# Optimization experiments

Hardware: AMD Instinct MI355X
Metric: run time of the kernel (lower is better)

## Reference

```python
import jax, jax.numpy as jnp
import numpy as np

B, S, D = 4, 2048, 1024
E, K, H = 8, 2, 2048  # experts, top_k, swiglu hidden (ff_multiplier=2.0)
EPS = 1e-8
RMS_EPS = 1e-6
ROPE_BASE = 10000.0


def setup_inputs() -> dict:
    key = jax.random.key(0)
    ks = jax.random.split(key, 6)
    scale_in = 1.0 / np.sqrt(D)
    scale_h = 1.0 / np.sqrt(H)
    return {
        "x": jax.random.normal(ks[0], (B, S, D), jnp.float32),
        "norm_w": jnp.ones((D,), jnp.float32),
        "router_W": jax.random.normal(ks[1], (E, D), jnp.float32) * scale_in,  # nn.Linear weight [E,D]
        "w1": jax.random.normal(ks[2], (E, H, D), jnp.float32) * scale_in,  # gate proj per expert
        "w3": jax.random.normal(ks[3], (E, H, D), jnp.float32) * scale_in,  # up proj per expert
        "w2": jax.random.normal(ks[4], (E, D, H), jnp.float32) * scale_h,   # down proj per expert
    }


def _rmsnorm(x, w):
    var = jnp.mean(jnp.square(x), axis=-1, keepdims=True)
    return x * jax.lax.rsqrt(var + RMS_EPS) * w


def _rope(x):
    # half-split rotary embedding over full embed dim; x: [B,S,D]
    d2 = D // 2
    inv_freq = 1.0 / (ROPE_BASE ** (jnp.arange(0, d2, dtype=jnp.float32) / d2))
    ang = jnp.arange(S, dtype=jnp.float32)[:, None] * inv_freq[None, :]  # [S,D/2]
    cos, sin = jnp.cos(ang), jnp.sin(ang)
    x1, x2 = x[..., :d2], x[..., d2:]
    return jnp.concatenate([x1 * cos - x2 * sin, x1 * sin + x2 * cos], axis=-1)


def reference(x, norm_w, router_W, w1, w3, w2):
    hidden = _rope(_rmsnorm(x, norm_w))  # [B,S,D]
    logits = jnp.einsum("bsd,ed->bse", hidden, router_W)
    probs = jax.nn.softmax(logits, axis=-1)
    # sparse top-k renormalized gates
    top_v, top_i = jax.lax.top_k(probs, K)  # [B,S,K]
    sparse = jnp.sum(jax.nn.one_hot(top_i, E, dtype=probs.dtype) * top_v[..., None], axis=-2)  # [B,S,E]
    gates = sparse / jnp.clip(jnp.sum(sparse, axis=-1, keepdims=True), EPS)
    # dense all-expert SwiGLU
    g = jnp.einsum("bsd,ehd->bseh", hidden, w1)
    u = jnp.einsum("bsd,ehd->bseh", hidden, w3)
    act = jax.nn.silu(g) * u
    expert_out = jnp.einsum("bseh,edh->bsed", act, w2)  # [B,S,E,D]
    mixed = jnp.sum(gates[..., None] * expert_out, axis=-2)
    return mixed + x
```

## Files before the change

kernel.cpp:

```cpp
#include <hip/hip_runtime.h>

#define TOKENS 8192
#define Dm 1024
#define Hm 2048
#define Sm 2048
#define D2 512
#define SLOTS 16384
#define PADU 256
#define SLOTPAD (SLOTS + 8*PADU)
#define NWE 16777216

#define OF_TAB 0ull
#define OF_HID (OF_TAB + (size_t)Sm*D2*8)
#define OF_ACT (OF_HID + (size_t)TOKENS*Dm*2)
#define OF_W1B (OF_ACT + (size_t)SLOTPAD*Hm*2)
#define OF_W3B (OF_W1B + (size_t)NWE*2)
#define OF_W2B (OF_W3B + (size_t)NWE*2)
#define OF_T2I (OF_W2B + (size_t)NWE*2)
#define OF_T2G (OF_T2I + (size_t)TOKENS*2*4)
#define OF_T2S (OF_T2G + (size_t)TOKENS*2*4)
#define OF_ST  (OF_T2S + (size_t)TOKENS*2*4)
#define OF_SG  (OF_ST + (size_t)SLOTPAD*4)
#define OF_MT  (OF_SG + (size_t)SLOTPAD*4)
#define OF_SO  (OF_MT + 1024)

#define PREP_TOKEN 8192
#define PREP_CONV  (PREP_TOKEN + 3 * (NWE / (256 * 8)))
#define PREP_INIT  (PREP_CONV + (SLOTPAD + 255) / 256)

typedef __bf16 bf16x8 __attribute__((ext_vector_type(8)));
typedef short  s16x8  __attribute__((ext_vector_type(8)));
typedef float  f32x4  __attribute__((ext_vector_type(4)));

__device__ __forceinline__ unsigned short f2bf(float f) {
    union { float f; unsigned u; } v; v.f = f;
    unsigned r = v.u + 0x7fffu + ((v.u >> 16) & 1u);
    return (unsigned short)(r >> 16);
}

__device__ __forceinline__ float bf2f(unsigned short u) {
    union { unsigned u; float f; } v; v.u = ((unsigned)u) << 16;
    return v.f;
}

__device__ __forceinline__ f32x4 mfma16(s16x8 a, s16x8 b, f32x4 c) {
    return __builtin_amdgcn_mfma_f32_16x16x32_bf16(
        __builtin_bit_cast(bf16x8, a), __builtin_bit_cast(bf16x8, b), c, 0, 0, 0);
}

__device__ __forceinline__ void gld16(const void* g, void* l) {
    __builtin_amdgcn_global_load_lds(
        (const __attribute__((address_space(1))) void*)g,
        (__attribute__((address_space(3))) void*)l, 16, 0, 0);
}

__device__ __forceinline__ int xcd_swz(int bid, int nwg) {
    int cpx = nwg >> 3;
    return (bid & 7) * cpx + (bid >> 3);
}

__global__ __launch_bounds__(256) void k_prep(
    const float* __restrict__ x, const float* __restrict__ nw,
    const float* __restrict__ rW,
    const float* __restrict__ w1, const float* __restrict__ w3,
    const float* __restrict__ w2,
    unsigned short* __restrict__ hid, int* __restrict__ t2i,
    float* __restrict__ t2g,
    unsigned short* __restrict__ d1, unsigned short* __restrict__ d3,
    unsigned short* __restrict__ d2,
    int* __restrict__ slot_token, int* __restrict__ meta)
{
    __shared__ float red[4];
    __shared__ float rl[4][8];
    int bid = blockIdx.x;
    int tid = threadIdx.x;

    if (bid >= PREP_CONV) {
        int i = (bid - PREP_CONV) * 256 + tid;
        if (i < SLOTPAD) slot_token[i] = -1;
        if (i < 8) meta[i] = 0;
        return;
    }
    if (bid >= PREP_TOKEN) {
        size_t i = ((size_t)(bid - PREP_TOKEN) * 256 + tid) * 8;
        const float* s; unsigned short* d;
        if (i < (size_t)NWE)            { s = w1; d = d1; }
        else if (i < 2ull * NWE)        { s = w3; d = d3; i -= (size_t)NWE; }
        else                            { s = w2; d = d2; i -= 2ull * NWE; }
        float4 a = *(const float4*)(s + i);
        float4 b = *(const float4*)(s + i + 4);
        s16x8 v;
        v[0]=(short)f2bf(a.x); v[1]=(short)f2bf(a.y); v[2]=(short)f2bf(a.z); v[3]=(short)f2bf(a.w);
        v[4]=(short)f2bf(b.x); v[5]=(short)f2bf(b.y); v[6]=(short)f2bf(b.z); v[7]=(short)f2bf(b.w);
        *(s16x8*)(d + i) = v;
        return;
    }

    int t = bid;
    int lane = tid & 63, wid = tid >> 6;
    int s = t & (Sm - 1);
    const float* xr = x + (size_t)t * Dm;

    float v0 = xr[tid], v1 = xr[tid + 256], v2 = xr[tid + 512], v3 = xr[tid + 768];
    float ss = v0*v0 + v1*v1 + v2*v2 + v3*v3;
    #pragma unroll
    for (int o = 32; o; o >>= 1) ss += __shfl_down(ss, o);
    if (lane == 0) red[wid] = ss;
    __syncthreads();
    float tot = red[0] + red[1] + red[2] + red[3];
    float rms = rsqrtf(tot * (1.0f / Dm) + 1e-6f);

    float n0 = v0 * rms * nw[tid];
    float n1 = v1 * rms * nw[tid + 256];
    float n2 = v2 * rms * nw[tid + 512];
    float n3 = v3 * rms * nw[tid + 768];

    const float kk = -0.017988946039016842f;
    float a0 = (float)s * expf((float)tid * kk);
    float a1 = (float)s * expf((float)(tid + 256) * kk);
    float c0x = cosf(a0), c0y = sinf(a0);
    float c1x = cosf(a1), c1y = sinf(a1);
    float h0 = n0 * c0x - n2 * c0y;
    float h2 = n0 * c0y + n2 * c0x;
    float h1 = n1 * c1x - n3 * c1y;
    float h3 = n1 * c1y + n3 * c1x;

    size_t base = (size_t)t * Dm;
    hid[base + tid]       = f2bf(h0);
    hid[base + tid + 256] = f2bf(h1);
    hid[base + tid + 512] = f2bf(h2);
    hid[base + tid + 768] = f2bf(h3);

    float p[8];
    #pragma unroll
    for (int e = 0; e < 8; e++) {
        const float* r = rW + (size_t)e * Dm;
        p[e] = h0 * r[tid] + h1 * r[tid + 256] + h2 * r[tid + 512] + h3 * r[tid + 768];
    }
    #pragma unroll
    for (int e = 0; e < 8; e++)
        #pragma unroll
        for (int o = 32; o; o >>= 1) p[e] += __shfl_down(p[e], o);
    if (lane == 0) {
        #pragma unroll
        for (int e = 0; e < 8; e++) rl[wid][e] = p[e];
    }
    __syncthreads();
    if (tid == 0) {
        float lg[8];
        #pragma unroll
        for (int e = 0; e < 8; e++) lg[e] = rl[0][e] + rl[1][e] + rl[2][e] + rl[3][e];
        float m = lg[0];
        #pragma unroll
        for (int e = 1; e < 8; e++) m = fmaxf(m, lg[e]);
        int i0 = 0; float b0 = lg[0];
        #pragma unroll
        for (int e = 1; e < 8; e++) if (lg[e] > b0) { b0 = lg[e]; i0 = e; }
        int i1 = -1; float b1 = -3.0e38f;
        #pragma unroll
        for (int e = 0; e < 8; e++) if (e != i0 && lg[e] > b1) { b1 = lg[e]; i1 = e; }
        float p0 = expf(b0 - m), p1 = expf(b1 - m);
        float inv = 1.0f / (p0 + p1);
        t2i[2 * t] = i0; t2i[2 * t + 1] = i1;
        t2g[2 * t] = p0 * inv; t2g[2 * t + 1] = p1 * inv;
    }
}

__global__ __launch_bounds__(256) void k_hist(const int* __restrict__ t2i,
                                              int* __restrict__ meta) {
    __shared__ int h[8];
    int tid = threadIdx.x;
    if (tid < 8) h[tid] = 0;
    __syncthreads();
    int base = blockIdx.x * 512 + tid * 2;
    atomicAdd(&h[t2i[base]], 1);
    atomicAdd(&h[t2i[base + 1]], 1);
    __syncthreads();
    if (tid < 8) atomicAdd(&meta[tid], h[tid]);
}

__global__ void k_offsets(int* meta) {
    if (threadIdx.x == 0 && blockIdx.x == 0) {
        int acc = 0;
        for (int e = 0; e < 8; e++) {
            meta[8 + e] = acc;
            acc += ((meta[e] + PADU - 1) / PADU) * PADU;
        }
        meta[16] = acc;
        for (int e = 0; e < 8; e++) meta[17 + e] = meta[8 + e];
    }
}

__global__ __launch_bounds__(256) void k_place(
    const int* __restrict__ t2i, const float* __restrict__ t2g,
    int* __restrict__ slot_token, float* __restrict__ slot_gate,
    int* __restrict__ t2s, int* __restrict__ meta)
{
    __shared__ int lcnt[8];
    __shared__ int lbase[8];
    int tid = threadIdx.x;
    if (tid < 8) lcnt[tid] = 0;
    __syncthreads();
    int t = blockIdx.x * 256 + tid;
    int e0 = t2i[2 * t], e1 = t2i[2 * t + 1];
    int r0 = atomicAdd(&lcnt[e0], 1);
    int r1 = atomicAdd(&lcnt[e1], 1);
    __syncthreads();
    if (tid < 8) lbase[tid] = atomicAdd(&meta[17 + tid], lcnt[tid]);
    __syncthreads();
    int p0 = lbase[e0] + r0, p1 = lbase[e1] + r1;
    slot_token[p0] = t; slot_gate[p0] = t2g[2 * t];     t2s[2 * t]     = p0;
    slot_token[p1] = t; slot_gate[p1] = t2g[2 * t + 1]; t2s[2 * t + 1] = p1;
}

__global__ __launch_bounds__(512) void k_gemm1(
    const unsigned short* __restrict__ hid,
    const unsigned short* __restrict__ w1b, const unsigned short* __restrict__ w3b,
    const int* __restrict__ slot_token, unsigned short* __restrict__ act,
    const int* __restrict__ meta)
{
    int nwg = gridDim.x * gridDim.y;
    int bid = blockIdx.y * gridDim.x + blockIdx.x;
    int wg  = xcd_swz(bid, nwg);
    int bx  = wg % gridDim.x, by = wg / gridDim.x;

    int row0 = by * 256;
    if (row0 >= meta[16]) return;
    int e = 0;
    #pragma unroll
    for (int q = 1; q < 8; q++) if (row0 >= meta[8 + q]) e = q;
    int h0 = bx * 128;

    __shared__ unsigned short As[2][256 * 64];
    __shared__ unsigned short Bs[2][256 * 64];

    int tid = threadIdx.x, lane = tid & 63, w = tid >> 6;
    int wm = w >> 2, wn = w & 3;
    int wrow = wm * 128, wcol = wn * 32;
    int frow = lane & 15, q4 = lane >> 4;
    int rx = frow & 7;

    int grow = tid >> 3;
    int sslot = (tid & 7) ^ (grow & 7);

    const unsigned short* srcA[4];
    const unsigned short* srcB[4];
    #pragma unroll
    for (int g = 0; g < 4; g++) {
        int ra = g * 64 + grow;
        int tok = slot_token[row0 + ra];  if (tok < 0) tok = 0;
        srcA[g] = hid + (size_t)tok * Dm + sslot * 8;
        int rb = g * 64 + grow;
        srcB[g] = (rb < 128 ? w1b + ((size_t)e * Hm + h0 + rb) * Dm
                            : w3b + ((size_t)e * Hm + h0 + rb - 128) * Dm) + sslot * 8;
    }

    s16x8 a8[4][2], bG[2][2], bU[2][2];
    f32x4 accG[8][2] = {};
    f32x4 accU[8][2] = {};

#define SA(nb, g) gld16(srcA[g] + koff, (unsigned short*)&As[(nb)][(g) * 4096 + tid * 8])
#define SB(nb, g) gld16(srcB[g] + koff, (unsigned short*)&Bs[(nb)][(g) * 4096 + tid * 8])

#define RD_A(buf, half) do {                                                  \
    _Pragma("unroll") for (int i_ = 0; i_ < 4; i_++)                          \
    _Pragma("unroll") for (int kh_ = 0; kh_ < 2; kh_++) {                     \
        int sp_ = ((kh_ << 2) | q4) ^ rx;                                     \
        a8[i_][kh_] = *(const s16x8*)&As[(buf)][(wrow + (half) * 64 + i_ * 16 + frow) * 64 + sp_ * 8]; \
    } } while (0)

#define RD_B(buf, arr, base) do {                                             \
    _Pragma("unroll") for (int j_ = 0; j_ < 2; j_++)                          \
    _Pragma("unroll") for (int kh_ = 0; kh_ < 2; kh_++) {                     \
        int sp_ = ((kh_ << 2) | q4) ^ rx;                                     \
        arr[j_][kh_] = *(const s16x8*)&Bs[(buf)][((base) + wcol + j_ * 16 + frow) * 64 + sp_ * 8]; \
    } } while (0)

#define MFMA_Q(accX, bX, half) do {                                           \
    _Pragma("unroll") for (int i_ = 0; i_ < 4; i_++)                          \
    _Pragma("unroll") for (int j_ = 0; j_ < 2; j_++)                          \
    _Pragma("unroll") for (int kh_ = 0; kh_ < 2; kh_++)                       \
        accX[(half) * 4 + i_][j_] = mfma16(a8[i_][kh_], bX[j_][kh_], accX[(half) * 4 + i_][j_]); \
    } while (0)

#define PH_PRE  do { __builtin_amdgcn_s_barrier();                            \
    asm volatile("s_waitcnt lgkmcnt(0)" ::: "memory");                        \
    __builtin_amdgcn_sched_barrier(0);                                        \
    __builtin_amdgcn_s_setprio(1); } while (0)
#define PH_POST do { __builtin_amdgcn_s_setprio(0);                           \
    __builtin_amdgcn_s_barrier(); } while (0)

    {
        int koff = 0;
        #pragma unroll
        for (int g = 0; g < 4; g++) SA(0, g);
        #pragma unroll
        for (int g = 0; g < 4; g++) SB(0, g);
        asm volatile("s_waitcnt vmcnt(0)" ::: "memory");
        __builtin_amdgcn_s_barrier();
    }

    for (int kt = 0; kt < 16; ++kt) {
        int buf = kt & 1, nbuf = buf ^ 1;
        int koff = (kt + 1) * 64;
        bool st = kt < 15;
        RD_A(buf, 0); RD_B(buf, bG, 0);
        if (st) { SA(nbuf, 0); SA(nbuf, 1); SA(nbuf, 2); }
        PH_PRE; MFMA_Q(accG, bG, 0); PH_POST;
        RD_B(buf, bU, 128);
        if (st) { SA(nbuf, 3); SB(nbuf, 0); SB(nbuf, 1); }
        PH_PRE; MFMA_Q(accU, bU, 0); PH_POST;
        RD_A(buf, 1);
        if (st) { SB(nbuf, 2); SB(nbuf, 3); }
        PH_PRE; MFMA_Q(accG, bG, 1); PH_POST;
        __builtin_amdgcn_s_setprio(1);
        MFMA_Q(accU, bU, 1);
        __builtin_amdgcn_s_setprio(0);
        asm volatile("s_waitcnt vmcnt(0)" ::: "memory");
        __builtin_amdgcn_s_barrier();
        __builtin_amdgcn_sched_barrier(0);
    }

#undef SA
#undef SB
#undef RD_A
#undef RD_B
#undef MFMA_Q
#undef PH_PRE
#undef PH_POST

    #pragma unroll
    for (int m = 0; m < 8; m++)
        #pragma unroll
        for (int j = 0; j < 2; j++)
            #pragma unroll
            for (int r = 0; r < 4; r++) {
                int sr = row0 + wrow + m * 16 + q4 * 4 + r;
                int hc = h0 + wcol + j * 16 + frow;
                float g = accG[m][j][r], u = accU[m][j][r];
                float a = g / (1.0f + expf(-g)) * u;
                act[(size_t)sr * Hm + hc] = f2bf(a);
            }
}

__global__ __launch_bounds__(256) void k_gemm2(
    const unsigned short* __restrict__ act, const unsigned short* __restrict__ w2b,
    const float* __restrict__ slot_gate,
    unsigned short* __restrict__ sout, const int* __restrict__ meta)
{
    int nwg = gridDim.x * gridDim.y;
    int bid = blockIdx.y * gridDim.x + blockIdx.x;
    int wg  = xcd_swz(bid, nwg);
    int bx  = wg % gridDim.x, by = wg / gridDim.x;

    int row0 = by * 128;
    if (row0 >= meta[16]) return;
    int e = 0;
    #pragma unroll
    for (int q = 1; q < 8; q++) if (row0 >= meta[8 + q]) e = q;
    int d0 = bx * 128;

    __shared__ unsigned short As[2][128 * 64];
    __shared__ unsigned short Bs[2][128 * 64];
    __shared__ float sgat[128];

    int tid = threadIdx.x, lane = tid & 63, w = tid >> 6;
    int wm = w >> 1, wn = w & 1;
    int frow = lane & 15, q4 = lane >> 4;
    int rx = frow & 7;

    if (tid < 128) sgat[tid] = slot_gate[row0 + tid];

    int r7 = (tid >> 3) & 7;
    int sslot = (tid & 7) ^ r7;

    const unsigned short* srcA[4];
    const unsigned short* srcB[4];
    #pragma unroll
    for (int i = 0; i < 4; i++) {
        int rr = i * 32 + (tid >> 3);
        srcA[i] = act + (size_t)(row0 + rr) * Hm + sslot * 8;
        srcB[i] = w2b + ((size_t)e * Dm + d0 + rr) * Hm + sslot * 8;
    }

    f32x4 acc[4][4] = {};

#define STAGE2(buf, k0) do {                                                  \
    unsigned short* la_ = &As[(buf)][tid * 8];                                \
    unsigned short* lb_ = &Bs[(buf)][tid * 8];                                \
    _Pragma("unroll")                                                         \
    for (int i_ = 0; i_ < 4; i_++) {                                          \
        gld16(srcA[i_] + (k0), la_ + i_ * 2048);                              \
        gld16(srcB[i_] + (k0), lb_ + i_ * 2048);                              \
    } } while (0)

#define COMP2(buf) do {                                                       \
    _Pragma("unroll")                                                         \
    for (int h_ = 0; h_ < 2; h_++) {                                          \
        int sp_ = ((h_ << 2) | q4) ^ rx;                                      \
        s16x8 am_[4], bn_[4];                                                 \
        _Pragma("unroll")                                                     \
        for (int i_ = 0; i_ < 4; i_++)                                        \
            am_[i_] = *(const s16x8*)&As[(buf)][(wm * 64 + i_ * 16 + frow) * 64 + sp_ * 8]; \
        _Pragma("unroll")                                                     \
        for (int j_ = 0; j_ < 4; j_++)                                        \
            bn_[j_] = *(const s16x8*)&Bs[(buf)][(wn * 64 + j_ * 16 + frow) * 64 + sp_ * 8]; \
        _Pragma("unroll")                                                     \
        for (int i_ = 0; i_ < 4; i_++)                                        \
            _Pragma("unroll")                                                 \
            for (int j_ = 0; j_ < 4; j_++)                                    \
                acc[i_][j_] = mfma16(am_[i_], bn_[j_], acc[i_][j_]);          \
    } } while (0)

    STAGE2(0, 0);
    #pragma unroll 2
    for (int kt = 0; kt < 31; ++kt) {
        STAGE2((kt + 1) & 1, (kt + 1) * 64);
        asm volatile("s_waitcnt vmcnt(8)" ::: "memory");
        __builtin_amdgcn_s_barrier();
        __builtin_amdgcn_sched_barrier(0);
        COMP2(kt & 1);
        __builtin_amdgcn_sched_barrier(0);
        __builtin_amdgcn_s_barrier();
    }
    asm volatile("s_waitcnt vmcnt(0)" ::: "memory");
    __builtin_amdgcn_s_barrier();
    __builtin_amdgcn_sched_barrier(0);
    COMP2(1);

#undef STAGE2
#undef COMP2

    #pragma unroll
    for (int i = 0; i < 4; i++) {
        #pragma unroll
        for (int r = 0; r < 4; r++) {
            int srl = wm * 64 + i * 16 + q4 * 4 + r;
            float gate = sgat[srl];
            size_t rb = (size_t)(row0 + srl) * Dm;
            #pragma unroll
            for (int j = 0; j < 4; j++) {
                int dc = d0 + wn * 64 + j * 16 + frow;
                sout[rb + dc] = f2bf(gate * acc[i][j][r]);
            }
        }
    }
}

__global__ __launch_bounds__(256) void k_final(
    const float* __restrict__ x, const unsigned short* __restrict__ sout,
    const int* __restrict__ t2s, float* __restrict__ out)
{
    int t = blockIdx.x;
    int tid = threadIdx.x;
    int s0 = t2s[2 * t], s1 = t2s[2 * t + 1];
    const float4*  xr = (const float4*)(x + (size_t)t * Dm);
    const ushort4* a  = (const ushort4*)(sout + (size_t)s0 * Dm);
    const ushort4* b  = (const ushort4*)(sout + (size_t)s1 * Dm);
    float4* o = (float4*)(out + (size_t)t * Dm);
    float4 xv = xr[tid];
    ushort4 av = a[tid], bv = b[tid];
    float4 r;
    r.x = xv.x + bf2f(av.x) + bf2f(bv.x);
    r.y = xv.y + bf2f(av.y) + bf2f(bv.y);
    r.z = xv.z + bf2f(av.z) + bf2f(bv.z);
    r.w = xv.w + bf2f(av.w) + bf2f(bv.w);
    o[tid] = r;
}

extern "C" void kernel_launch(void* const* d_in, const int* in_sizes, int n_in,
                              void* d_out, int out_size, void* d_ws, size_t ws_size,
                              hipStream_t stream) {
    const float* x  = (const float*)d_in[0];
    const float* nw = (const float*)d_in[1];
    const float* rW = (const float*)d_in[2];
    const float* w1 = (const float*)d_in[3];
    const float* w3 = (const float*)d_in[4];
    const float* w2 = (const float*)d_in[5];
    float* out = (float*)d_out;
    char* ws = (char*)d_ws;

    unsigned short* hid = (unsigned short*)(ws + OF_HID);
    unsigned short* act = (unsigned short*)(ws + OF_ACT);
    unsigned short* w1b = (unsigned short*)(ws + OF_W1B);
    unsigned short* w3b = (unsigned short*)(ws + OF_W3B);
    unsigned short* w2b = (unsigned short*)(ws + OF_W2B);
    int*   t2i  = (int*)(ws + OF_T2I);
    float* t2g  = (float*)(ws + OF_T2G);
    int*   t2s  = (int*)(ws + OF_T2S);
    int*   stok = (int*)(ws + OF_ST);
    float* sgat = (float*)(ws + OF_SG);
    int*   meta = (int*)(ws + OF_MT);
    unsigned short* sout = (unsigned short*)(ws + OF_SO);

    k_prep<<<PREP_INIT, 256, 0, stream>>>(x, nw, rW, w1, w3, w2,
                                          hid, t2i, t2g, w1b, w3b, w2b,
                                          stok, meta);
    k_hist<<<32, 256, 0, stream>>>(t2i, meta);
    k_offsets<<<1, 64, 0, stream>>>(meta);
    k_place<<<TOKENS / 256, 256, 0, stream>>>(t2i, t2g, stok, sgat, t2s, meta);

    dim3 g1(Hm / 128, SLOTPAD / 256);
    k_gemm1<<<g1, 512, 0, stream>>>(hid, w1b, w3b, stok, act, meta);
    dim3 g2(Dm / 128, SLOTPAD / 128);
    k_gemm2<<<g2, 256, 0, stream>>>(act, w2b, sgat, sout, meta);
    k_final<<<TOKENS, 256, 0, stream>>>(x, sout, t2s, out);
}
```

Measured before the change: 370.2 us.

## Use 32x32 MFMA in gemm1 and move w2 conversion into gemm1 tail blocks

Switches the gate/up GEMM from 16x16x32 bf16 MFMA tiles to 32x32x16 tiles, reshaping the LDS fragment reads and the epilogue row mapping to match. This gives more work per instruction and fewer LDS fragment loads. It also moves the fp32-to-bf16 conversion of w2 out of the prep kernel into extra blocks appended to the gemm1 grid, so that conversion can overlap with the GEMM tail. The risks are register pressure from the 16-wide accumulators and a 1D grid whose trailing conversion blocks may compete with GEMM blocks for compute units.

```diff
diff --git a/kernel.cpp b/kernel.cpp
--- a/kernel.cpp
+++ b/kernel.cpp
@@ -25,12 +25,19 @@
 #define OF_SO  (OF_MT + 1024)
 
 #define PREP_TOKEN 8192
-#define PREP_CONV  (PREP_TOKEN + 3 * (NWE / (256 * 8)))
+#define PREP_CONV  (PREP_TOKEN + 2 * (NWE / (256 * 8)))
 #define PREP_INIT  (PREP_CONV + (SLOTPAD + 255) / 256)
+
+#define G1_GX   (Hm / 128)
+#define G1_GY   (SLOTPAD / 256)
+#define G1_BLKS (G1_GX * G1_GY)
+#define G1_CONV (NWE / (512 * 8))
+#define G1_TOT  (G1_BLKS + G1_CONV)
 
 typedef __bf16 bf16x8 __attribute__((ext_vector_type(8)));
 typedef short  s16x8  __attribute__((ext_vector_type(8)));
 typedef float  f32x4  __attribute__((ext_vector_type(4)));
+typedef float  f32x16 __attribute__((ext_vector_type(16)));
 
 __device__ __forceinline__ unsigned short f2bf(float f) {
     union { float f; unsigned u; } v; v.f = f;
@@ -48,6 +55,11 @@
         __builtin_bit_cast(bf16x8, a), __builtin_bit_cast(bf16x8, b), c, 0, 0, 0);
 }
 
+__device__ __forceinline__ f32x16 mfma32(s16x8 a, s16x8 b, f32x16 c) {
+    return __builtin_amdgcn_mfma_f32_32x32x16_bf16(
+        __builtin_bit_cast(bf16x8, a), __builtin_bit_cast(bf16x8, b), c, 0, 0, 0);
+}
+
 __device__ __forceinline__ void gld16(const void* g, void* l) {
     __builtin_amdgcn_global_load_lds(
         (const __attribute__((address_space(1))) void*)g,
@@ -63,11 +75,9 @@
     const float* __restrict__ x, const float* __restrict__ nw,
     const float* __restrict__ rW,
     const float* __restrict__ w1, const float* __restrict__ w3,
-    const float* __restrict__ w2,
     unsigned short* __restrict__ hid, int* __restrict__ t2i,
     float* __restrict__ t2g,
     unsigned short* __restrict__ d1, unsigned short* __restrict__ d3,
-    unsigned short* __restrict__ d2,
     int* __restrict__ slot_token, int* __restrict__ meta)
 {
     __shared__ float red[4];
@@ -84,9 +94,8 @@
     if (bid >= PREP_TOKEN) {
         size_t i = ((size_t)(bid - PREP_TOKEN) * 256 + tid) * 8;
         const float* s; unsigned short* d;
-        if (i < (size_t)NWE)            { s = w1; d = d1; }
-        else if (i < 2ull * NWE)        { s = w3; d = d3; i -= (size_t)NWE; }
-        else                            { s = w2; d = d2; i -= 2ull * NWE; }
+        if (i < (size_t)NWE) { s = w1; d = d1; }
+        else                 { s = w3; d = d3; i -= (size_t)NWE; }
         float4 a = *(const float4*)(s + i);
         float4 b = *(const float4*)(s + i + 4);
         s16x8 v;
@@ -217,12 +226,24 @@
     const unsigned short* __restrict__ hid,
     const unsigned short* __restrict__ w1b, const unsigned short* __restrict__ w3b,
     const int* __restrict__ slot_token, unsigned short* __restrict__ act,
-    const int* __restrict__ meta)
+    const int* __restrict__ meta,
+    const float* __restrict__ w2, unsigned short* __restrict__ w2b)
 {
-    int nwg = gridDim.x * gridDim.y;
-    int bid = blockIdx.y * gridDim.x + blockIdx.x;
-    int wg  = xcd_swz(bid, nwg);
-    int bx  = wg % gridDim.x, by = wg / gridDim.x;
+    int bid0 = blockIdx.x;
+    int tid = threadIdx.x;
+    if (bid0 >= G1_BLKS) {
+        size_t i = ((size_t)(bid0 - G1_BLKS) * 512 + tid) * 8;
+        float4 a = *(const float4*)(w2 + i);
+        float4 b = *(const float4*)(w2 + i + 4);
+        s16x8 v;
+        v[0]=(short)f2bf(a.x); v[1]=(short)f2bf(a.y); v[2]=(short)f2bf(a.z); v[3]=(short)f2bf(a.w);
+        v[4]=(short)f2bf(b.x); v[5]=(short)f2bf(b.y); v[6]=(short)f2bf(b.z); v[7]=(short)f2bf(b.w);
+        *(s16x8*)(w2b + i) = v;
+        return;
+    }
+
+    int wg  = xcd_swz(bid0, G1_BLKS);
+    int bx  = wg % G1_GX, by = wg / G1_GX;
 
     int row0 = by * 256;
     if (row0 >= meta[16]) return;
@@ -234,11 +255,11 @@
     __shared__ unsigned short As[2][256 * 64];
     __shared__ unsigned short Bs[2][256 * 64];
 
-    int tid = threadIdx.x, lane = tid & 63, w = tid >> 6;
+    int lane = tid & 63, w = tid >> 6;
     int wm = w >> 2, wn = w & 3;
     int wrow = wm * 128, wcol = wn * 32;
-    int frow = lane & 15, q4 = lane >> 4;
-    int rx = frow & 7;
+    int l31 = lane & 31, kh = lane >> 5;
+    int rx = lane & 7;
 
     int grow = tid >> 3;
     int sslot = (tid & 7) ^ (grow & 7);
@@ -255,32 +276,30 @@
                             : w3b + ((size_t)e * Hm + h0 + rb - 128) * Dm) + sslot * 8;
     }
 
-    s16x8 a8[4][2], bG[2][2], bU[2][2];
-    f32x4 accG[8][2] = {};
-    f32x4 accU[8][2] = {};
+    s16x8 a8[2][4], bG[4], bU[4];
+    f32x16 accG[4] = {};
+    f32x16 accU[4] = {};
 
 #define SA(nb, g) gld16(srcA[g] + koff, (unsigned short*)&As[(nb)][(g) * 4096 + tid * 8])
 #define SB(nb, g) gld16(srcB[g] + koff, (unsigned short*)&Bs[(nb)][(g) * 4096 + tid * 8])
 
 #define RD_A(buf, half) do {                                                  \
-    _Pragma("unroll") for (int i_ = 0; i_ < 4; i_++)                          \
-    _Pragma("unroll") for (int kh_ = 0; kh_ < 2; kh_++) {                     \
-        int sp_ = ((kh_ << 2) | q4) ^ rx;                                     \
-        a8[i_][kh_] = *(const s16x8*)&As[(buf)][(wrow + (half) * 64 + i_ * 16 + frow) * 64 + sp_ * 8]; \
+    _Pragma("unroll") for (int mt_ = 0; mt_ < 2; mt_++)                       \
+    _Pragma("unroll") for (int ks_ = 0; ks_ < 4; ks_++) {                     \
+        int sp_ = ((ks_ << 1) | kh) ^ rx;                                     \
+        a8[mt_][ks_] = *(const s16x8*)&As[(buf)][(wrow + (half) * 64 + mt_ * 32 + l31) * 64 + sp_ * 8]; \
     } } while (0)
 
 #define RD_B(buf, arr, base) do {                                             \
-    _Pragma("unroll") for (int j_ = 0; j_ < 2; j_++)                          \
-    _Pragma("unroll") for (int kh_ = 0; kh_ < 2; kh_++) {                     \
-        int sp_ = ((kh_ << 2) | q4) ^ rx;                                     \
-        arr[j_][kh_] = *(const s16x8*)&Bs[(buf)][((base) + wcol + j_ * 16 + frow) * 64 + sp_ * 8]; \
+    _Pragma("unroll") for (int ks_ = 0; ks_ < 4; ks_++) {                     \
+        int sp_ = ((ks_ << 1) | kh) ^ rx;                                     \
+        arr[ks_] = *(const s16x8*)&Bs[(buf)][((base) + wcol + l31) * 64 + sp_ * 8]; \
     } } while (0)
 
 #define MFMA_Q(accX, bX, half) do {                                           \
-    _Pragma("unroll") for (int i_ = 0; i_ < 4; i_++)                          \
-    _Pragma("unroll") for (int j_ = 0; j_ < 2; j_++)                          \
-    _Pragma("unroll") for (int kh_ = 0; kh_ < 2; kh_++)                       \
-        accX[(half) * 4 + i_][j_] = mfma16(a8[i_][kh_], bX[j_][kh_], accX[(half) * 4 + i_][j_]); \
+    _Pragma("unroll") for (int mt_ = 0; mt_ < 2; mt_++)                       \
+    _Pragma("unroll") for (int ks_ = 0; ks_ < 4; ks_++)                       \
+        accX[(half) * 2 + mt_] = mfma32(a8[mt_][ks_], bX[ks_], accX[(half) * 2 + mt_]); \
     } while (0)
 
 #define PH_PRE  do { __builtin_amdgcn_s_barrier();                            \
@@ -330,17 +349,15 @@
 #undef PH_POST
 
     #pragma unroll
-    for (int m = 0; m < 8; m++)
-        #pragma unroll
-        for (int j = 0; j < 2; j++)
-            #pragma unroll
-            for (int r = 0; r < 4; r++) {
-                int sr = row0 + wrow + m * 16 + q4 * 4 + r;
-                int hc = h0 + wcol + j * 16 + frow;
-                float g = accG[m][j][r], u = accU[m][j][r];
-                float a = g / (1.0f + expf(-g)) * u;
-                act[(size_t)sr * Hm + hc] = f2bf(a);
-            }
+    for (int q = 0; q < 4; q++)
+        #pragma unroll
+        for (int r = 0; r < 16; r++) {
+            int sr = row0 + wrow + q * 32 + (r & 3) + 8 * (r >> 2) + 4 * kh;
+            int hc = h0 + wcol + l31;
+            float g = accG[q][r], u = accU[q][r];
+            float a = g / (1.0f + expf(-g)) * u;
+            act[(size_t)sr * Hm + hc] = f2bf(a);
+        }
 }
 
 __global__ __launch_bounds__(256) void k_gemm2(
@@ -493,15 +510,14 @@
     int*   meta = (int*)(ws + OF_MT);
     unsigned short* sout = (unsigned short*)(ws + OF_SO);
 
-    k_prep<<<PREP_INIT, 256, 0, stream>>>(x, nw, rW, w1, w3, w2,
-                                          hid, t2i, t2g, w1b, w3b, w2b,
+    k_prep<<<PREP_INIT, 256, 0, stream>>>(x, nw, rW, w1, w3,
+                                          hid, t2i, t2g, w1b, w3b,
                                           stok, meta);
     k_hist<<<32, 256, 0, stream>>>(t2i, meta);
     k_offsets<<<1, 64, 0, stream>>>(meta);
     k_place<<<TOKENS / 256, 256, 0, stream>>>(t2i, t2g, stok, sgat, t2s, meta);
 
-    dim3 g1(Hm / 128, SLOTPAD / 256);
-    k_gemm1<<<g1, 512, 0, stream>>>(hid, w1b, w3b, stok, act, meta);
+    k_gemm1<<<G1_TOT, 512, 0, stream>>>(hid, w1b, w3b, stok, act, meta, w2, w2b);
     dim3 g2(Dm / 128, SLOTPAD / 128);
     k_gemm2<<<g2, 256, 0, stream>>>(act, w2b, sgat, sout, meta);
     k_final<<<TOKENS, 256, 0, stream>>>(x, sout, t2s, out);
```

Result: no change. 377.1 us (+1.9%).
